# Kernel optimization log

Hardware: AMD Instinct MI355X
Metric: run time of the kernel (lower is better)

Reference implementation:

```python
import jax, jax.numpy as jnp
import numpy as np

EMBED_DIM = 1024
NUM_HEADS = 16
HEAD_DIM = EMBED_DIM // NUM_HEADS


def setup_inputs() -> dict:
    key = jax.random.key(0)
    ks = jax.random.split(key, 10)
    B, S, D = 4, 2048, EMBED_DIM
    s = 1.0 / np.sqrt(D)
    return {
        "x": jax.random.normal(ks[0], (B, S, D), dtype=jnp.float32),
        "Wq": jax.random.normal(ks[1], (D, D), dtype=jnp.float32) * s,
        "bq": jnp.zeros((D,), dtype=jnp.float32),
        "Wk": jax.random.normal(ks[2], (D, D), dtype=jnp.float32) * s,
        "bk": jnp.zeros((D,), dtype=jnp.float32),
        "Wv": jax.random.normal(ks[3], (D, D), dtype=jnp.float32) * s,
        "bv": jnp.zeros((D,), dtype=jnp.float32),
        "Wo": jax.random.normal(ks[4], (D, D), dtype=jnp.float32) * s,
        "bo": jnp.zeros((D,), dtype=jnp.float32),
        "ln_w": jnp.ones((D,), dtype=jnp.float32),
        "ln_b": jnp.zeros((D,), dtype=jnp.float32),
    }


def _layernorm(x, w, b, eps=1e-5):
    mu = jnp.mean(x, axis=-1, keepdims=True)
    var = jnp.mean(jnp.square(x - mu), axis=-1, keepdims=True)
    return (x - mu) * jax.lax.rsqrt(var + eps) * w + b


def reference(x, Wq, bq, Wk, bk, Wv, bv, Wo, bo, ln_w, ln_b):
    B, S, D = x.shape
    H, hd = NUM_HEADS, HEAD_DIM
    # projections (torch Linear: x @ W.T + b)
    q = (x @ Wq.T + bq).reshape(B, S, H, hd).transpose(0, 2, 1, 3)  # [B,H,S,hd]
    k = (x @ Wk.T + bk).reshape(B, S, H, hd).transpose(0, 2, 1, 3)
    v = (x @ Wv.T + bv).reshape(B, S, H, hd).transpose(0, 2, 1, 3)
    scores = jnp.einsum("bhqd,bhkd->bhqk", q, k) / np.sqrt(hd)
    attn = jax.nn.softmax(scores, axis=-1)
    out = jnp.einsum("bhqk,bhkd->bhqd", attn, v)
    out = out.transpose(0, 2, 1, 3).reshape(B, S, D)
    out = out @ Wo.T + bo
    return _layernorm(out, ln_w, ln_b)
```

## Files before the change

kernel.cpp:

```cpp
#include <hip/hip_runtime.h>
#include <hip/hip_bf16.h>
#include <math.h>

typedef unsigned short u16;
typedef unsigned int   u32;
typedef short bf16x8 __attribute__((ext_vector_type(8)));
typedef float f32x4  __attribute__((ext_vector_type(4)));
typedef float f32x16 __attribute__((ext_vector_type(16)));
typedef u32   u32x4  __attribute__((ext_vector_type(4)));

#define B_   4
#define S_   2048
#define D_   1024
#define H_   16
#define HD_  64
#define M_   (B_*S_)

static __device__ __forceinline__ u16 f2bf(float f) {
  __hip_bfloat16 h = __float2bfloat16(f);
  return *reinterpret_cast<u16*>(&h);
}
static __device__ __forceinline__ u32 pack_bf(float lo, float hi) {
  return (u32)f2bf(lo) | ((u32)f2bf(hi) << 16);
}
static __device__ __forceinline__ u32 pack_bf_trunc(float lo, float hi) {
  return __builtin_amdgcn_perm(__float_as_uint(hi), __float_as_uint(lo), 0x07060302u);
}
static __device__ __forceinline__ f32x16 zero16() {
  f32x16 z;
#pragma unroll
  for (int i = 0; i < 16; ++i) z[i] = 0.f;
  return z;
}

typedef __attribute__((address_space(1))) const u32* gas_t;
typedef __attribute__((address_space(3))) u32* las_t;
static __device__ __forceinline__ void g2l16(const void* g, void* l) {
  __builtin_amdgcn_global_load_lds((gas_t)g, (las_t)l, 16, 0, 0);
}

__global__ __launch_bounds__(256) void cast_all(const float* __restrict__ x,
                                                const float* __restrict__ Wq,
                                                const float* __restrict__ Wk,
                                                const float* __restrict__ Wv,
                                                const float* __restrict__ Wo,
                                                u16* __restrict__ xb,
                                                u16* __restrict__ Wqb,
                                                u16* __restrict__ Wkb,
                                                u16* __restrict__ Wvb,
                                                u16* __restrict__ Wob) {
  int bid = blockIdx.x;
  const float* src;
  u16* dst;
  int off;
  if (bid < 8192) {
    src = x; dst = xb; off = bid;
  } else {
    int t = bid - 8192;
    int w = t >> 10;
    off   = t & 1023;
    src = w == 0 ? Wq : w == 1 ? Wk : w == 2 ? Wv : Wo;
    dst = w == 0 ? Wqb : w == 1 ? Wkb : w == 2 ? Wvb : Wob;
  }
  int i = (off * 256 + threadIdx.x) * 4;
  float4 v = *reinterpret_cast<const float4*>(src + i);
  uint2 o;
  o.x = pack_bf(v.x, v.y);
  o.y = pack_bf(v.z, v.w);
  *reinterpret_cast<uint2*>(dst + i) = o;
}

__global__ __launch_bounds__(256) void gemm_qkv(const u16* __restrict__ A,
                                                const u16* __restrict__ Wq,
                                                const u16* __restrict__ Wk,
                                                const u16* __restrict__ Wv,
                                                const float* __restrict__ bq,
                                                const float* __restrict__ bk,
                                                const float* __restrict__ bv,
                                                u16* __restrict__ Qo,
                                                u16* __restrict__ Ko,
                                                u16* __restrict__ Vo) {
  const int tid  = threadIdx.x;
  const int lane = tid & 63;
  const int wave = tid >> 6;
  const int m16  = lane & 15;
  const int quad = lane >> 4;
  const int wm   = wave & 1;
  const int wn   = wave >> 1;
  const int which = blockIdx.x % 3;
  const int m0   = (blockIdx.x / 3) * 128;
  const int n0   = blockIdx.y * 128;

  const u16* W = which == 0 ? Wq : which == 1 ? Wk : Wv;
  const float* bias = which == 0 ? bq : which == 1 ? bk : bv;

  __shared__ __align__(16) u16 As[128 * 32];
  __shared__ __align__(16) u16 Bs[128 * 32];

  f32x4 acc[4][4];
#pragma unroll
  for (int i = 0; i < 4; ++i)
#pragma unroll
    for (int j = 0; j < 4; ++j) acc[i][j] = (f32x4){0.f, 0.f, 0.f, 0.f};

  for (int k0 = 0; k0 < 1024; k0 += 32) {
#pragma unroll
    for (int i = 0; i < 2; ++i) {
      int e0  = i * 256 + (wave << 6);
      int e   = e0 + lane;
      int row = e >> 2;
      int c8  = (e & 3) * 8;
      g2l16(&A[(size_t)(m0 + row) * 1024 + k0 + c8], &As[e0 * 8]);
      g2l16(&W[(size_t)(n0 + row) * 1024 + k0 + c8], &Bs[e0 * 8]);
    }
    __syncthreads();

    bf16x8 af[4], bfr[4];
#pragma unroll
    for (int mt = 0; mt < 4; ++mt)
      af[mt] = *reinterpret_cast<const bf16x8*>(&As[(wm * 64 + mt * 16 + m16) * 32 + quad * 8]);
#pragma unroll
    for (int nt = 0; nt < 4; ++nt)
      bfr[nt] = *reinterpret_cast<const bf16x8*>(&Bs[(wn * 64 + nt * 16 + m16) * 32 + quad * 8]);

#pragma unroll
    for (int mt = 0; mt < 4; ++mt)
#pragma unroll
      for (int nt = 0; nt < 4; ++nt)
        acc[mt][nt] = __builtin_amdgcn_mfma_f32_16x16x32_bf16(af[mt], bfr[nt], acc[mt][nt], 0, 0, 0);
    __syncthreads();
  }

  const float scale = which == 0 ? 0.125f * 1.44269504f : 1.0f;
  u16* ob = which == 0 ? Qo : which == 1 ? Ko : Vo;
#pragma unroll
  for (int mt = 0; mt < 4; ++mt) {
#pragma unroll
    for (int nt = 0; nt < 4; ++nt) {
      int col = n0 + wn * 64 + nt * 16 + m16;
      float bi = bias[col];
      int row0 = m0 + wm * 64 + mt * 16 + quad * 4;
      int b = row0 >> 11, s = row0 & 2047;
      int h = col >> 6,  d = col & 63;
      float v[4];
#pragma unroll
      for (int r = 0; r < 4; ++r) v[r] = (acc[mt][nt][r] + bi) * scale;
      if (which < 2) {
#pragma unroll
        for (int r = 0; r < 4; ++r)
          ob[(size_t)((b * H_ + h) * S_ + s + r) * HD_ + d] = f2bf(v[r]);
      } else {
        uint2 w;
        w.x = pack_bf(v[0], v[1]);
        w.y = pack_bf(v[2], v[3]);
        *reinterpret_cast<uint2*>(&ob[(size_t)((b * H_ + h) * HD_ + d) * S_ + s]) = w;
      }
    }
  }
}

__global__ __launch_bounds__(256) void gemm_bt(const u16* __restrict__ A,
                                               const u16* __restrict__ W,
                                               const float* __restrict__ bias,
                                               float* __restrict__ out) {
  const int tid  = threadIdx.x;
  const int lane = tid & 63;
  const int wave = tid >> 6;
  const int m16  = lane & 15;
  const int quad = lane >> 4;
  const int wm   = wave & 1;
  const int wn   = wave >> 1;
  const int m0   = blockIdx.x * 128;
  const int n0   = blockIdx.y * 128;

  __shared__ __align__(16) u16 As[128 * 32];
  __shared__ __align__(16) u16 Bs[128 * 32];

  f32x4 acc[4][4];
#pragma unroll
  for (int i = 0; i < 4; ++i)
#pragma unroll
    for (int j = 0; j < 4; ++j) acc[i][j] = (f32x4){0.f, 0.f, 0.f, 0.f};

  for (int k0 = 0; k0 < 1024; k0 += 32) {
#pragma unroll
    for (int i = 0; i < 2; ++i) {
      int e0  = i * 256 + (wave << 6);
      int e   = e0 + lane;
      int row = e >> 2;
      int c8  = (e & 3) * 8;
      g2l16(&A[(size_t)(m0 + row) * 1024 + k0 + c8], &As[e0 * 8]);
      g2l16(&W[(size_t)(n0 + row) * 1024 + k0 + c8], &Bs[e0 * 8]);
    }
    __syncthreads();

    bf16x8 af[4], bfr[4];
#pragma unroll
    for (int mt = 0; mt < 4; ++mt)
      af[mt] = *reinterpret_cast<const bf16x8*>(&As[(wm * 64 + mt * 16 + m16) * 32 + quad * 8]);
#pragma unroll
    for (int nt = 0; nt < 4; ++nt)
      bfr[nt] = *reinterpret_cast<const bf16x8*>(&Bs[(wn * 64 + nt * 16 + m16) * 32 + quad * 8]);

#pragma unroll
    for (int mt = 0; mt < 4; ++mt)
#pragma unroll
      for (int nt = 0; nt < 4; ++nt)
        acc[mt][nt] = __builtin_amdgcn_mfma_f32_16x16x32_bf16(af[mt], bfr[nt], acc[mt][nt], 0, 0, 0);
    __syncthreads();
  }

#pragma unroll
  for (int mt = 0; mt < 4; ++mt) {
#pragma unroll
    for (int nt = 0; nt < 4; ++nt) {
      int col = n0 + wn * 64 + nt * 16 + m16;
      float bi = bias[col];
#pragma unroll
      for (int r = 0; r < 4; ++r) {
        int row = m0 + wm * 64 + mt * 16 + quad * 4 + r;
        out[(size_t)row * 1024 + col] = acc[mt][nt][r] + bi;
      }
    }
  }
}

__global__ __launch_bounds__(256, 4) void attn_kernel(const u16* __restrict__ Q,
                                                      const u16* __restrict__ K,
                                                      const u16* __restrict__ Vt,
                                                      u16* __restrict__ out) {
  const int tid  = threadIdx.x;
  const int lane = tid & 63;
  const int wave = tid >> 6;
  const int r32  = lane & 31;
  const int h32  = lane >> 5;
  const int bh   = blockIdx.y;
  const int q0   = blockIdx.x * 128 + wave * 32;

  __shared__ __align__(16) u16 Ks[64 * 72];
  __shared__ __align__(16) u16 Vs[64 * 72];

  const u16* kbase = K  + (size_t)bh * S_ * HD_;
  const u16* vbase = Vt + (size_t)bh * HD_ * S_;
  const int e  = tid;
  const int e2 = tid + 256;
  const int row_a = e >> 3,  c8_a = (e & 7) * 8;
  const int row_b = e2 >> 3, c8_b = (e2 & 7) * 8;

  bf16x8 qf[4];
  {
    const u16* qbase = Q + (size_t)(bh * S_ + q0 + r32) * HD_ + h32 * 8;
#pragma unroll
    for (int dc = 0; dc < 4; ++dc)
      qf[dc] = *reinterpret_cast<const bf16x8*>(qbase + dc * 16);
  }

  f32x16 acc[2];
#pragma unroll
  for (int dt = 0; dt < 2; ++dt) acc[dt] = zero16();
  float lsum = 0.f;

  uint4 kr0 = *reinterpret_cast<const uint4*>(&kbase[(size_t)row_a * HD_ + c8_a]);
  uint4 kr1 = *reinterpret_cast<const uint4*>(&kbase[(size_t)row_b * HD_ + c8_b]);
  uint4 vr0 = *reinterpret_cast<const uint4*>(&vbase[(size_t)row_a * S_ + c8_a]);
  uint4 vr1 = *reinterpret_cast<const uint4*>(&vbase[(size_t)row_b * S_ + c8_b]);

  const int NT = S_ / 64;
  for (int kt = 0; kt < NT; ++kt) {
    *reinterpret_cast<uint4*>(&Ks[row_a * 72 + c8_a]) = kr0;
    *reinterpret_cast<uint4*>(&Ks[row_b * 72 + c8_b]) = kr1;
    *reinterpret_cast<uint4*>(&Vs[row_a * 72 + c8_a]) = vr0;
    *reinterpret_cast<uint4*>(&Vs[row_b * 72 + c8_b]) = vr1;
    __syncthreads();

    {
      const int kn = (kt + 1 < NT ? kt + 1 : kt) * 64;
      kr0 = *reinterpret_cast<const uint4*>(&kbase[(size_t)(kn + row_a) * HD_ + c8_a]);
      kr1 = *reinterpret_cast<const uint4*>(&kbase[(size_t)(kn + row_b) * HD_ + c8_b]);
      vr0 = *reinterpret_cast<const uint4*>(&vbase[(size_t)row_a * S_ + kn + c8_a]);
      vr1 = *reinterpret_cast<const uint4*>(&vbase[(size_t)row_b * S_ + kn + c8_b]);
    }

    f32x16 sc[2];
#pragma unroll
    for (int nt = 0; nt < 2; ++nt) {
      sc[nt] = zero16();
#pragma unroll
      for (int dc = 0; dc < 4; ++dc) {
        bf16x8 kf = *reinterpret_cast<const bf16x8*>(&Ks[(nt * 32 + r32) * 72 + dc * 16 + h32 * 8]);
        sc[nt] = __builtin_amdgcn_mfma_f32_32x32x16_bf16(kf, qf[dc], sc[nt], 0, 0, 0);
      }
    }

    u32 pk[2][8];
    float ps = 0.f;
#pragma unroll
    for (int nt = 0; nt < 2; ++nt)
#pragma unroll
      for (int i = 0; i < 8; ++i) {
        float p0 = __builtin_amdgcn_exp2f(sc[nt][2 * i]);
        float p1 = __builtin_amdgcn_exp2f(sc[nt][2 * i + 1]);
        ps += p0 + p1;
        pk[nt][i] = pack_bf_trunc(p0, p1);
      }
    lsum += ps;

#pragma unroll
    for (int nt = 0; nt < 2; ++nt) {
#pragma unroll
      for (int kc2 = 0; kc2 < 2; ++kc2) {
        u32 s0 = h32 ? pk[nt][4 * kc2 + 0] : pk[nt][4 * kc2 + 2];
        u32 s1 = h32 ? pk[nt][4 * kc2 + 1] : pk[nt][4 * kc2 + 3];
        u32 x0 = (u32)__shfl_xor((int)s0, 32);
        u32 x1 = (u32)__shfl_xor((int)s1, 32);
        u32x4 bw;
        bw[0] = h32 ? x0 : pk[nt][4 * kc2 + 0];
        bw[1] = h32 ? x1 : pk[nt][4 * kc2 + 1];
        bw[2] = h32 ? pk[nt][4 * kc2 + 2] : x0;
        bw[3] = h32 ? pk[nt][4 * kc2 + 3] : x1;
        bf16x8 pfrag = *reinterpret_cast<bf16x8*>(&bw);
        const int kc = nt * 2 + kc2;
#pragma unroll
        for (int dt = 0; dt < 2; ++dt) {
          bf16x8 vf = *reinterpret_cast<const bf16x8*>(&Vs[(dt * 32 + r32) * 72 + kc * 16 + h32 * 8]);
          acc[dt] = __builtin_amdgcn_mfma_f32_32x32x16_bf16(vf, pfrag, acc[dt], 0, 0, 0);
        }
      }
    }
    __syncthreads();
  }

  const int b = bh >> 4, hh = bh & 15;
  float lt  = lsum + __shfl_xor(lsum, 32);
  float inv = 1.f / lt;
  int srow = q0 + r32;
  u16* orow = out + (size_t)(b * S_ + srow) * D_ + hh * HD_;
#pragma unroll
  for (int dt = 0; dt < 2; ++dt) {
#pragma unroll
    for (int g = 0; g < 4; ++g) {
      uint2 w;
      w.x = pack_bf(acc[dt][4 * g + 0] * inv, acc[dt][4 * g + 1] * inv);
      w.y = pack_bf(acc[dt][4 * g + 2] * inv, acc[dt][4 * g + 3] * inv);
      *reinterpret_cast<uint2*>(orow + dt * 32 + 8 * g + 4 * h32) = w;
    }
  }
}

__global__ __launch_bounds__(256) void ln_kernel(const float* __restrict__ X,
                                                 const float* __restrict__ w,
                                                 const float* __restrict__ b,
                                                 float* __restrict__ out) {
  const int row = blockIdx.x;
  const int tid = threadIdx.x;
  const float* x = X + (size_t)row * 1024;
  float vals[4];
  float s = 0.f, s2 = 0.f;
#pragma unroll
  for (int i = 0; i < 4; ++i) {
    float v = x[tid + i * 256];
    vals[i] = v;
    s += v;
    s2 += v * v;
  }
#pragma unroll
  for (int off = 32; off; off >>= 1) {
    s  += __shfl_xor(s, off);
    s2 += __shfl_xor(s2, off);
  }
  __shared__ float a1[4], a2[4];
  if ((tid & 63) == 0) { a1[tid >> 6] = s; a2[tid >> 6] = s2; }
  __syncthreads();
  s  = a1[0] + a1[1] + a1[2] + a1[3];
  s2 = a2[0] + a2[1] + a2[2] + a2[3];
  float mu  = s * (1.f / 1024.f);
  float var = s2 * (1.f / 1024.f) - mu * mu;
  float inv = rsqrtf(var + 1e-5f);
#pragma unroll
  for (int i = 0; i < 4; ++i) {
    int c = tid + i * 256;
    out[(size_t)row * 1024 + c] = (vals[i] - mu) * inv * w[c] + b[c];
  }
}

extern "C" void kernel_launch(void* const* d_in, const int* in_sizes, int n_in,
                              void* d_out, int out_size, void* d_ws, size_t ws_size,
                              hipStream_t stream) {
  const float* x   = (const float*)d_in[0];
  const float* Wq  = (const float*)d_in[1];
  const float* bq  = (const float*)d_in[2];
  const float* Wk  = (const float*)d_in[3];
  const float* bk  = (const float*)d_in[4];
  const float* Wv  = (const float*)d_in[5];
  const float* bv  = (const float*)d_in[6];
  const float* Wo  = (const float*)d_in[7];
  const float* bo  = (const float*)d_in[8];
  const float* lnw = (const float*)d_in[9];
  const float* lnb = (const float*)d_in[10];

  const size_t MB = 1024ull * 1024ull;
  char* ws = (char*)d_ws;
  u16* xb  = (u16*)(ws + 0);
  u16* Qb  = (u16*)(ws + 16 * MB);
  u16* Kb  = (u16*)(ws + 32 * MB);
  u16* Vtb = (u16*)(ws + 48 * MB);
  u16* Wqb = (u16*)(ws + 64 * MB);
  u16* Wkb = (u16*)(ws + 66 * MB);
  u16* Wvb = (u16*)(ws + 68 * MB);
  u16* Wob = (u16*)(ws + 70 * MB);
  float* Of = (float*)(ws + 16 * MB);

  cast_all<<<8192 + 4096, 256, 0, stream>>>(x, Wq, Wk, Wv, Wo, xb, Wqb, Wkb, Wvb, Wob);

  gemm_qkv<<<dim3((M_ / 128) * 3, D_ / 128), 256, 0, stream>>>(
      xb, Wqb, Wkb, Wvb, bq, bk, bv, Qb, Kb, Vtb);

  attn_kernel<<<dim3(S_ / 128, B_ * H_), 256, 0, stream>>>(Qb, Kb, Vtb, xb);

  gemm_bt<<<dim3(M_ / 128, D_ / 128), 256, 0, stream>>>(xb, Wob, bo, Of);

  ln_kernel<<<M_, 256, 0, stream>>>(Of, lnw, lnb, (float*)d_out);
}
```

Baseline: 303.9 us.

## Double-buffer attention K/V tiles and vectorize GEMM epilogue stores via swapped MFMA operands

The attention kernel now uses two LDS buffers for K/V tiles and a two-step unrolled loop, so staging the next tile overlaps compute on the current one and one barrier per tile is dropped. In the QKV and output-projection GEMMs the MFMA operands are swapped so each lane holds four consecutive columns. This lets the epilogues write packed bf16 uint2 or float4 values instead of scattered scalar stores. The costs are doubled LDS in attention, which may reduce occupancy, and more register pressure from holding two sets of prefetch registers.

Measured after the change: 319.3 us. +5.1%, slower.

```diff
diff --git a/kernel.cpp b/kernel.cpp
--- a/kernel.cpp
+++ b/kernel.cpp
@@ -123,36 +123,57 @@
     for (int nt = 0; nt < 4; ++nt)
       bfr[nt] = *reinterpret_cast<const bf16x8*>(&Bs[(wn * 64 + nt * 16 + m16) * 32 + quad * 8]);
 
-#pragma unroll
-    for (int mt = 0; mt < 4; ++mt)
-#pragma unroll
-      for (int nt = 0; nt < 4; ++nt)
-        acc[mt][nt] = __builtin_amdgcn_mfma_f32_16x16x32_bf16(af[mt], bfr[nt], acc[mt][nt], 0, 0, 0);
+    if (which < 2) {
+#pragma unroll
+      for (int mt = 0; mt < 4; ++mt)
+#pragma unroll
+        for (int nt = 0; nt < 4; ++nt)
+          acc[mt][nt] = __builtin_amdgcn_mfma_f32_16x16x32_bf16(bfr[nt], af[mt], acc[mt][nt], 0, 0, 0);
+    } else {
+#pragma unroll
+      for (int mt = 0; mt < 4; ++mt)
+#pragma unroll
+        for (int nt = 0; nt < 4; ++nt)
+          acc[mt][nt] = __builtin_amdgcn_mfma_f32_16x16x32_bf16(af[mt], bfr[nt], acc[mt][nt], 0, 0, 0);
+    }
     __syncthreads();
   }
 
   const float scale = which == 0 ? 0.125f * 1.44269504f : 1.0f;
   u16* ob = which == 0 ? Qo : which == 1 ? Ko : Vo;
-#pragma unroll
-  for (int mt = 0; mt < 4; ++mt) {
+  if (which < 2) {
 #pragma unroll
     for (int nt = 0; nt < 4; ++nt) {
-      int col = n0 + wn * 64 + nt * 16 + m16;
-      float bi = bias[col];
-      int row0 = m0 + wm * 64 + mt * 16 + quad * 4;
-      int b = row0 >> 11, s = row0 & 2047;
-      int h = col >> 6,  d = col & 63;
-      float v[4];
-#pragma unroll
-      for (int r = 0; r < 4; ++r) v[r] = (acc[mt][nt][r] + bi) * scale;
-      if (which < 2) {
-#pragma unroll
-        for (int r = 0; r < 4; ++r)
-          ob[(size_t)((b * H_ + h) * S_ + s + r) * HD_ + d] = f2bf(v[r]);
-      } else {
+      int nb = n0 + wn * 64 + nt * 16 + quad * 4;
+      float4 b4 = *reinterpret_cast<const float4*>(&bias[nb]);
+      int h = nb >> 6, d0 = nb & 63;
+#pragma unroll
+      for (int mt = 0; mt < 4; ++mt) {
+        int m = m0 + wm * 64 + mt * 16 + m16;
+        int b = m >> 11, s = m & 2047;
+        float v0 = (acc[mt][nt][0] + b4.x) * scale;
+        float v1 = (acc[mt][nt][1] + b4.y) * scale;
+        float v2 = (acc[mt][nt][2] + b4.z) * scale;
+        float v3 = (acc[mt][nt][3] + b4.w) * scale;
         uint2 w;
-        w.x = pack_bf(v[0], v[1]);
-        w.y = pack_bf(v[2], v[3]);
+        w.x = pack_bf(v0, v1);
+        w.y = pack_bf(v2, v3);
+        *reinterpret_cast<uint2*>(&ob[(size_t)((b * H_ + h) * S_ + s) * HD_ + d0]) = w;
+      }
+    }
+  } else {
+#pragma unroll
+    for (int mt = 0; mt < 4; ++mt) {
+#pragma unroll
+      for (int nt = 0; nt < 4; ++nt) {
+        int col = n0 + wn * 64 + nt * 16 + m16;
+        float bi = bias[col];
+        int row0 = m0 + wm * 64 + mt * 16 + quad * 4;
+        int b = row0 >> 11, s = row0 & 2047;
+        int h = col >> 6,  d = col & 63;
+        uint2 w;
+        w.x = pack_bf(acc[mt][nt][0] + bi, acc[mt][nt][1] + bi);
+        w.y = pack_bf(acc[mt][nt][2] + bi, acc[mt][nt][3] + bi);
         *reinterpret_cast<uint2*>(&ob[(size_t)((b * H_ + h) * HD_ + d) * S_ + s]) = w;
       }
     }
@@ -206,21 +227,74 @@
     for (int mt = 0; mt < 4; ++mt)
 #pragma unroll
       for (int nt = 0; nt < 4; ++nt)
-        acc[mt][nt] = __builtin_amdgcn_mfma_f32_16x16x32_bf16(af[mt], bfr[nt], acc[mt][nt], 0, 0, 0);
-    __syncthreads();
-  }
-
-#pragma unroll
-  for (int mt = 0; mt < 4; ++mt) {
-#pragma unroll
-    for (int nt = 0; nt < 4; ++nt) {
-      int col = n0 + wn * 64 + nt * 16 + m16;
-      float bi = bias[col];
-#pragma unroll
-      for (int r = 0; r < 4; ++r) {
-        int row = m0 + wm * 64 + mt * 16 + quad * 4 + r;
-        out[(size_t)row * 1024 + col] = acc[mt][nt][r] + bi;
-      }
+        acc[mt][nt] = __builtin_amdgcn_mfma_f32_16x16x32_bf16(bfr[nt], af[mt], acc[mt][nt], 0, 0, 0);
+    __syncthreads();
+  }
+
+#pragma unroll
+  for (int nt = 0; nt < 4; ++nt) {
+    int nb = n0 + wn * 64 + nt * 16 + quad * 4;
+    float4 b4 = *reinterpret_cast<const float4*>(&bias[nb]);
+#pragma unroll
+    for (int mt = 0; mt < 4; ++mt) {
+      int m = m0 + wm * 64 + mt * 16 + m16;
+      float4 o;
+      o.x = acc[mt][nt][0] + b4.x;
+      o.y = acc[mt][nt][1] + b4.y;
+      o.z = acc[mt][nt][2] + b4.z;
+      o.w = acc[mt][nt][3] + b4.w;
+      *reinterpret_cast<float4*>(&out[(size_t)m * 1024 + nb]) = o;
+    }
+  }
+}
+
+static __device__ __forceinline__ void attn_compute(const u16* __restrict__ ks,
+                                                    const u16* __restrict__ vs,
+                                                    const bf16x8 qf[4],
+                                                    int r32, int h32,
+                                                    f32x16& a0, f32x16& a1,
+                                                    float& lsum) {
+  f32x16 sc[2];
+#pragma unroll
+  for (int nt = 0; nt < 2; ++nt) {
+    sc[nt] = zero16();
+#pragma unroll
+    for (int dc = 0; dc < 4; ++dc) {
+      bf16x8 kf = *reinterpret_cast<const bf16x8*>(&ks[(nt * 32 + r32) * 72 + dc * 16 + h32 * 8]);
+      sc[nt] = __builtin_amdgcn_mfma_f32_32x32x16_bf16(kf, qf[dc], sc[nt], 0, 0, 0);
+    }
+  }
+  u32 pk[2][8];
+  float ps = 0.f;
+#pragma unroll
+  for (int nt = 0; nt < 2; ++nt)
+#pragma unroll
+    for (int i = 0; i < 8; ++i) {
+      float p0 = __builtin_amdgcn_exp2f(sc[nt][2 * i]);
+      float p1 = __builtin_amdgcn_exp2f(sc[nt][2 * i + 1]);
+      ps += p0 + p1;
+      pk[nt][i] = pack_bf_trunc(p0, p1);
+    }
+  lsum += ps;
+#pragma unroll
+  for (int nt = 0; nt < 2; ++nt) {
+#pragma unroll
+    for (int kc2 = 0; kc2 < 2; ++kc2) {
+      u32 s0 = h32 ? pk[nt][4 * kc2 + 0] : pk[nt][4 * kc2 + 2];
+      u32 s1 = h32 ? pk[nt][4 * kc2 + 1] : pk[nt][4 * kc2 + 3];
+      u32 x0 = (u32)__shfl_xor((int)s0, 32);
+      u32 x1 = (u32)__shfl_xor((int)s1, 32);
+      u32x4 bw;
+      bw[0] = h32 ? x0 : pk[nt][4 * kc2 + 0];
+      bw[1] = h32 ? x1 : pk[nt][4 * kc2 + 1];
+      bw[2] = h32 ? pk[nt][4 * kc2 + 2] : x0;
+      bw[3] = h32 ? pk[nt][4 * kc2 + 3] : x1;
+      bf16x8 pfrag = *reinterpret_cast<bf16x8*>(&bw);
+      const int kc = nt * 2 + kc2;
+      bf16x8 vf0 = *reinterpret_cast<const bf16x8*>(&vs[(r32) * 72 + kc * 16 + h32 * 8]);
+      bf16x8 vf1 = *reinterpret_cast<const bf16x8*>(&vs[(32 + r32) * 72 + kc * 16 + h32 * 8]);
+      a0 = __builtin_amdgcn_mfma_f32_32x32x16_bf16(vf0, pfrag, a0, 0, 0, 0);
+      a1 = __builtin_amdgcn_mfma_f32_32x32x16_bf16(vf1, pfrag, a1, 0, 0, 0);
     }
   }
 }
@@ -237,15 +311,14 @@
   const int bh   = blockIdx.y;
   const int q0   = blockIdx.x * 128 + wave * 32;
 
-  __shared__ __align__(16) u16 Ks[64 * 72];
-  __shared__ __align__(16) u16 Vs[64 * 72];
+  __shared__ __align__(16) u16 Ks[2][64 * 72];
+  __shared__ __align__(16) u16 Vs[2][64 * 72];
 
   const u16* kbase = K  + (size_t)bh * S_ * HD_;
   const u16* vbase = Vt + (size_t)bh * HD_ * S_;
-  const int e  = tid;
-  const int e2 = tid + 256;
-  const int row_a = e >> 3,  c8_a = (e & 7) * 8;
-  const int row_b = e2 >> 3, c8_b = (e2 & 7) * 8;
+  const int ra = tid >> 3;
+  const int rb = ra + 32;
+  const int ca = (tid & 7) * 8;
 
   bf16x8 qf[4];
   {
@@ -255,77 +328,50 @@
       qf[dc] = *reinterpret_cast<const bf16x8*>(qbase + dc * 16);
   }
 
-  f32x16 acc[2];
-#pragma unroll
-  for (int dt = 0; dt < 2; ++dt) acc[dt] = zero16();
+  f32x16 a0 = zero16(), a1 = zero16();
   float lsum = 0.f;
 
-  uint4 kr0 = *reinterpret_cast<const uint4*>(&kbase[(size_t)row_a * HD_ + c8_a]);
-  uint4 kr1 = *reinterpret_cast<const uint4*>(&kbase[(size_t)row_b * HD_ + c8_b]);
-  uint4 vr0 = *reinterpret_cast<const uint4*>(&vbase[(size_t)row_a * S_ + c8_a]);
-  uint4 vr1 = *reinterpret_cast<const uint4*>(&vbase[(size_t)row_b * S_ + c8_b]);
+  uint4 k0a = *reinterpret_cast<const uint4*>(&kbase[(size_t)ra * HD_ + ca]);
+  uint4 k0b = *reinterpret_cast<const uint4*>(&kbase[(size_t)rb * HD_ + ca]);
+  uint4 v0a = *reinterpret_cast<const uint4*>(&vbase[(size_t)ra * S_ + ca]);
+  uint4 v0b = *reinterpret_cast<const uint4*>(&vbase[(size_t)rb * S_ + ca]);
+  *reinterpret_cast<uint4*>(&Ks[0][ra * 72 + ca]) = k0a;
+  *reinterpret_cast<uint4*>(&Ks[0][rb * 72 + ca]) = k0b;
+  *reinterpret_cast<uint4*>(&Vs[0][ra * 72 + ca]) = v0a;
+  *reinterpret_cast<uint4*>(&Vs[0][rb * 72 + ca]) = v0b;
+  uint4 k1a = *reinterpret_cast<const uint4*>(&kbase[(size_t)(64 + ra) * HD_ + ca]);
+  uint4 k1b = *reinterpret_cast<const uint4*>(&kbase[(size_t)(64 + rb) * HD_ + ca]);
+  uint4 v1a = *reinterpret_cast<const uint4*>(&vbase[(size_t)ra * S_ + 64 + ca]);
+  uint4 v1b = *reinterpret_cast<const uint4*>(&vbase[(size_t)rb * S_ + 64 + ca]);
+  __syncthreads();
 
   const int NT = S_ / 64;
-  for (int kt = 0; kt < NT; ++kt) {
-    *reinterpret_cast<uint4*>(&Ks[row_a * 72 + c8_a]) = kr0;
-    *reinterpret_cast<uint4*>(&Ks[row_b * 72 + c8_b]) = kr1;
-    *reinterpret_cast<uint4*>(&Vs[row_a * 72 + c8_a]) = vr0;
-    *reinterpret_cast<uint4*>(&Vs[row_b * 72 + c8_b]) = vr1;
-    __syncthreads();
-
+  for (int kt = 0; kt < NT; kt += 2) {
+    attn_compute(Ks[0], Vs[0], qf, r32, h32, a0, a1, lsum);
+    *reinterpret_cast<uint4*>(&Ks[1][ra * 72 + ca]) = k1a;
+    *reinterpret_cast<uint4*>(&Ks[1][rb * 72 + ca]) = k1b;
+    *reinterpret_cast<uint4*>(&Vs[1][ra * 72 + ca]) = v1a;
+    *reinterpret_cast<uint4*>(&Vs[1][rb * 72 + ca]) = v1b;
     {
-      const int kn = (kt + 1 < NT ? kt + 1 : kt) * 64;
-      kr0 = *reinterpret_cast<const uint4*>(&kbase[(size_t)(kn + row_a) * HD_ + c8_a]);
-      kr1 = *reinterpret_cast<const uint4*>(&kbase[(size_t)(kn + row_b) * HD_ + c8_b]);
-      vr0 = *reinterpret_cast<const uint4*>(&vbase[(size_t)row_a * S_ + kn + c8_a]);
-      vr1 = *reinterpret_cast<const uint4*>(&vbase[(size_t)row_b * S_ + kn + c8_b]);
-    }
-
-    f32x16 sc[2];
-#pragma unroll
-    for (int nt = 0; nt < 2; ++nt) {
-      sc[nt] = zero16();
-#pragma unroll
-      for (int dc = 0; dc < 4; ++dc) {
-        bf16x8 kf = *reinterpret_cast<const bf16x8*>(&Ks[(nt * 32 + r32) * 72 + dc * 16 + h32 * 8]);
-        sc[nt] = __builtin_amdgcn_mfma_f32_32x32x16_bf16(kf, qf[dc], sc[nt], 0, 0, 0);
-      }
-    }
-
-    u32 pk[2][8];
-    float ps = 0.f;
-#pragma unroll
-    for (int nt = 0; nt < 2; ++nt)
-#pragma unroll
-      for (int i = 0; i < 8; ++i) {
-        float p0 = __builtin_amdgcn_exp2f(sc[nt][2 * i]);
-        float p1 = __builtin_amdgcn_exp2f(sc[nt][2 * i + 1]);
-        ps += p0 + p1;
-        pk[nt][i] = pack_bf_trunc(p0, p1);
-      }
-    lsum += ps;
-
-#pragma unroll
-    for (int nt = 0; nt < 2; ++nt) {
-#pragma unroll
-      for (int kc2 = 0; kc2 < 2; ++kc2) {
-        u32 s0 = h32 ? pk[nt][4 * kc2 + 0] : pk[nt][4 * kc2 + 2];
-        u32 s1 = h32 ? pk[nt][4 * kc2 + 1] : pk[nt][4 * kc2 + 3];
-        u32 x0 = (u32)__shfl_xor((int)s0, 32);
-        u32 x1 = (u32)__shfl_xor((int)s1, 32);
-        u32x4 bw;
-        bw[0] = h32 ? x0 : pk[nt][4 * kc2 + 0];
-        bw[1] = h32 ? x1 : pk[nt][4 * kc2 + 1];
-        bw[2] = h32 ? pk[nt][4 * kc2 + 2] : x0;
-        bw[3] = h32 ? pk[nt][4 * kc2 + 3] : x1;
-        bf16x8 pfrag = *reinterpret_cast<bf16x8*>(&bw);
-        const int kc = nt * 2 + kc2;
-#pragma unroll
-        for (int dt = 0; dt < 2; ++dt) {
-          bf16x8 vf = *reinterpret_cast<const bf16x8*>(&Vs[(dt * 32 + r32) * 72 + kc * 16 + h32 * 8]);
-          acc[dt] = __builtin_amdgcn_mfma_f32_32x32x16_bf16(vf, pfrag, acc[dt], 0, 0, 0);
-        }
-      }
+      int kn = (kt + 2 < NT ? kt + 2 : NT - 1) * 64;
+      k0a = *reinterpret_cast<const uint4*>(&kbase[(size_t)(kn + ra) * HD_ + ca]);
+      k0b = *reinterpret_cast<const uint4*>(&kbase[(size_t)(kn + rb) * HD_ + ca]);
+      v0a = *reinterpret_cast<const uint4*>(&vbase[(size_t)ra * S_ + kn + ca]);
+      v0b = *reinterpret_cast<const uint4*>(&vbase[(size_t)rb * S_ + kn + ca]);
+    }
+    __syncthreads();
+
+    attn_compute(Ks[1], Vs[1], qf, r32, h32, a0, a1, lsum);
+    *reinterpret_cast<uint4*>(&Ks[0][ra * 72 + ca]) = k0a;
+    *reinterpret_cast<uint4*>(&Ks[0][rb * 72 + ca]) = k0b;
+    *reinterpret_cast<uint4*>(&Vs[0][ra * 72 + ca]) = v0a;
+    *reinterpret_cast<uint4*>(&Vs[0][rb * 72 + ca]) = v0b;
+    {
+      int kn = (kt + 3 < NT ? kt + 3 : NT - 1) * 64;
+      k1a = *reinterpret_cast<const uint4*>(&kbase[(size_t)(kn + ra) * HD_ + ca]);
+      k1b = *reinterpret_cast<const uint4*>(&kbase[(size_t)(kn + rb) * HD_ + ca]);
+      v1a = *reinterpret_cast<const uint4*>(&vbase[(size_t)ra * S_ + kn + ca]);
+      v1b = *reinterpret_cast<const uint4*>(&vbase[(size_t)rb * S_ + kn + ca]);
     }
     __syncthreads();
   }
@@ -336,14 +382,14 @@
   int srow = q0 + r32;
   u16* orow = out + (size_t)(b * S_ + srow) * D_ + hh * HD_;
 #pragma unroll
-  for (int dt = 0; dt < 2; ++dt) {
-#pragma unroll
-    for (int g = 0; g < 4; ++g) {
-      uint2 w;
-      w.x = pack_bf(acc[dt][4 * g + 0] * inv, acc[dt][4 * g + 1] * inv);
-      w.y = pack_bf(acc[dt][4 * g + 2] * inv, acc[dt][4 * g + 3] * inv);
-      *reinterpret_cast<uint2*>(orow + dt * 32 + 8 * g + 4 * h32) = w;
-    }
+  for (int g = 0; g < 4; ++g) {
+    uint2 w;
+    w.x = pack_bf(a0[4 * g + 0] * inv, a0[4 * g + 1] * inv);
+    w.y = pack_bf(a0[4 * g + 2] * inv, a0[4 * g + 3] * inv);
+    *reinterpret_cast<uint2*>(orow + 8 * g + 4 * h32) = w;
+    w.x = pack_bf(a1[4 * g + 0] * inv, a1[4 * g + 1] * inv);
+    w.y = pack_bf(a1[4 * g + 2] * inv, a1[4 * g + 3] * inv);
+    *reinterpret_cast<uint2*>(orow + 32 + 8 * g + 4 * h32) = w;
   }
 }
 
```
